# Optimization experiments

Measured on AMD Instinct MI355X. Metric: run time of the kernel, lower is better.

## Reference

```python
import jax, jax.numpy as jnp
import numpy as np

EPS = 1e-12  # torch F.normalize default eps
DN = ('NCHW', 'OIHW', 'NCHW')

def _conv(x, w, groups=1):
    return jax.lax.conv_general_dilated(x, w, window_strides=(1, 1), padding='SAME',
                                        feature_group_count=groups, dimension_numbers=DN)

def setup_inputs() -> dict:
    key = jax.random.key(0)
    k1, k2, k3, k4 = jax.random.split(key, 4)
    b, c, h, w = 4, 64, 64, 64
    x = jax.random.normal(k1, (b, c, h, w), dtype=jnp.float32)
    w_qkv = jax.random.normal(k2, (3 * c, c, 1, 1), dtype=jnp.float32) * (1.0 / np.sqrt(c))
    w_dw = jax.random.normal(k3, (3 * c, 1, 3, 3), dtype=jnp.float32) * (1.0 / 3.0)
    w_proj = jax.random.normal(k4, (c, c, 3, 3), dtype=jnp.float32) * (1.0 / np.sqrt(9 * c))
    return {"x": x, "w_qkv": w_qkv, "w_dw": w_dw, "w_proj": w_proj}

def _l2norm(t):
    # torch F.normalize(dim=-1): t / max(||t||_2, eps)
    n = jnp.sqrt(jnp.sum(t * t, axis=-1, keepdims=True))
    return t / jnp.maximum(n, EPS)

def reference(x, w_qkv, w_dw, w_proj):
    b, c, h, w = x.shape
    qkv = _conv(_conv(x, w_qkv), w_dw, groups=3 * c)  # (b, 3c, h, w)
    q, k, v = jnp.split(qkv, 3, axis=1)
    hw = h * w
    q = _l2norm(q.reshape(b, c, hw))  # normalize each channel's spatial vector
    k = _l2norm(k.reshape(b, c, hw))
    v = v.reshape(b, c, hw)
    attn = jnp.einsum('bcn,bcm->bnm', q, k)        # (b, hw, hw) cosine scores
    attn = jax.nn.softmax(attn, axis=-1)
    out = jnp.einsum('bcm,bmn->bcn', v, attn)       # v @ attn
    out = out.reshape(b, c, h, w)
    return _conv(out, w_proj)
```

## Files before the change

kernel.cpp:

```cpp
#include <hip/hip_runtime.h>
#include <hip/hip_bf16.h>

typedef __attribute__((ext_vector_type(8))) short bf16x8;
typedef __attribute__((ext_vector_type(4))) float f32x4;
typedef __attribute__((ext_vector_type(8))) unsigned short ushort8;

#define HW 4096
#define NC 64
#define PROWS 4356

static __device__ __forceinline__ unsigned short f2bf(float f) {
    unsigned int u = __float_as_uint(f);
    unsigned int r = (u + 0x7FFFu + ((u >> 16) & 1u)) >> 16;
    return (unsigned short)r;
}

__global__ __launch_bounds__(256) void k_conv1x1(const float* __restrict__ x,
                                                 const float* __restrict__ wqkv,
                                                 float* __restrict__ out) {
    __shared__ float wl[512];
    int nb = blockIdx.x, ocg = blockIdx.y, b = blockIdx.z;
    int t = threadIdx.x;
    for (int i = t; i < 512; i += 256) wl[i] = wqkv[ocg * 512 + i];
    __syncthreads();
    int n = nb * 256 + t;
    const float* xb = x + (size_t)b * NC * HW + n;
    float acc[8] = {0.f,0.f,0.f,0.f,0.f,0.f,0.f,0.f};
    for (int ic = 0; ic < 64; ic++) {
        float xv = xb[(size_t)ic * HW];
        #pragma unroll
        for (int o = 0; o < 8; o++) acc[o] += wl[o * 64 + ic] * xv;
    }
    float* ob = out + (size_t)b * 192 * HW + (size_t)(ocg * 8) * HW + n;
    #pragma unroll
    for (int o = 0; o < 8; o++) ob[(size_t)o * HW] = acc[o];
}

__global__ __launch_bounds__(256) void k_dwconv(const float* __restrict__ in,
                                                const float* __restrict__ wdw,
                                                float* __restrict__ out) {
    int yg = blockIdx.x, ch = blockIdx.y, b = blockIdx.z;
    int t = threadIdx.x;
    int y = yg * 4 + (t >> 6), xx = t & 63;
    const float* ib = in + ((size_t)b * 192 + ch) * HW;
    const float* wp = wdw + ch * 9;
    float s = 0.f;
    #pragma unroll
    for (int dy = 0; dy < 3; dy++) {
        int yy = y + dy - 1;
        if (yy < 0 || yy > 63) continue;
        const float* r = ib + yy * 64;
        float v0 = (xx > 0) ? r[xx - 1] : 0.f;
        float v1 = r[xx];
        float v2 = (xx < 63) ? r[xx + 1] : 0.f;
        const float* wr = wp + dy * 3;
        s += wr[0] * v0 + wr[1] * v1 + wr[2] * v2;
    }
    out[((size_t)b * 192 + ch) * HW + y * 64 + xx] = s;
}

__global__ __launch_bounds__(256) void k_norms(const float* __restrict__ qkv,
                                               float* __restrict__ invn) {
    int ch = blockIdx.x, b = blockIdx.y;
    const float* p = qkv + ((size_t)b * 192 + ch) * HW;
    float s = 0.f;
    for (int i = threadIdx.x; i < HW; i += 256) { float v = p[i]; s += v * v; }
    #pragma unroll
    for (int m = 1; m < 64; m <<= 1) s += __shfl_xor(s, m);
    __shared__ float red[4];
    if ((threadIdx.x & 63) == 0) red[threadIdx.x >> 6] = s;
    __syncthreads();
    if (threadIdx.x == 0) {
        float tot = red[0] + red[1] + red[2] + red[3];
        float nrm = sqrtf(tot);
        invn[b * 128 + ch] = 1.f / fmaxf(nrm, 1e-12f);
    }
}

__global__ __launch_bounds__(256) void k_pack(const float* __restrict__ qkv,
                                              const float* __restrict__ invn,
                                              unsigned short* __restrict__ qT,
                                              unsigned short* __restrict__ kT,
                                              unsigned short* __restrict__ vn) {
    int nb = blockIdx.x, sel = blockIdx.y, b = blockIdx.z;
    int n = nb * 256 + threadIdx.x;
    if (sel == 2) {
        const float* src = qkv + ((size_t)b * 192 + 128) * HW + n;
        unsigned short* dst = vn + (size_t)b * NC * HW + n;
        for (int c = 0; c < 64; c++) dst[(size_t)c * HW] = f2bf(src[(size_t)c * HW]);
    } else {
        const float* src = qkv + ((size_t)b * 192 + sel * 64) * HW + n;
        const float* iv = invn + b * 128 + sel * 64;
        unsigned short* dst = (sel == 0 ? qT : kT) + ((size_t)b * HW + n) * NC;
        for (int c0 = 0; c0 < 64; c0 += 8) {
            ushort8 pk;
            #pragma unroll
            for (int j = 0; j < 8; j++)
                pk[j] = f2bf(src[(size_t)(c0 + j) * HW] * iv[c0 + j]);
            *reinterpret_cast<ushort8*>(dst + c0) = pk;
        }
    }
}

__global__ __launch_bounds__(256) void k_rowsum(const unsigned short* __restrict__ qT,
                                                const unsigned short* __restrict__ kT,
                                                float* __restrict__ part) {
    __shared__ __align__(16) unsigned short klds[2][64 * 72];
    int mblk = blockIdx.x, ns = blockIdx.y, b = blockIdx.z;
    int t = threadIdx.x;
    int w = t >> 6, lane = t & 63, g = lane >> 4, r15 = lane & 15;
    const unsigned short* qb = qT + (size_t)b * HW * NC;
    const unsigned short* kb = kT + (size_t)b * HW * NC;
    int m0 = mblk * 128 + w * 16;
    const unsigned short* qp0 = qb + (size_t)(m0 + r15) * NC + g * 8;
    const unsigned short* qp1 = qb + (size_t)(m0 + 64 + r15) * NC + g * 8;
    bf16x8 a0 = *reinterpret_cast<const bf16x8*>(qp0);
    bf16x8 a1 = *reinterpret_cast<const bf16x8*>(qp0 + 32);
    bf16x8 a2 = *reinterpret_cast<const bf16x8*>(qp1);
    bf16x8 a3 = *reinterpret_cast<const bf16x8*>(qp1 + 32);
    float sa[4] = {0.f, 0.f, 0.f, 0.f};
    float sb[4] = {0.f, 0.f, 0.f, 0.f};
    int nbase = ns * 512;
    int n_loc = t >> 2, seg = t & 3;
    {
        const unsigned short* sp = kb + (size_t)(nbase + n_loc) * NC + seg * 16;
        *reinterpret_cast<ushort8*>(&klds[0][n_loc * 72 + seg * 16]) = *reinterpret_cast<const ushort8*>(sp);
        *reinterpret_cast<ushort8*>(&klds[0][n_loc * 72 + seg * 16 + 8]) = *reinterpret_cast<const ushort8*>(sp + 8);
    }
    __syncthreads();
    int cur = 0;
    for (int it = 0; it < 8; it++) {
        ushort8 r0, r1;
        bool hasnext = it < 7;
        if (hasnext) {
            const unsigned short* sp = kb + (size_t)(nbase + (it + 1) * 64 + n_loc) * NC + seg * 16;
            r0 = *reinterpret_cast<const ushort8*>(sp);
            r1 = *reinterpret_cast<const ushort8*>(sp + 8);
        }
        #pragma unroll
        for (int tt = 0; tt < 4; tt++) {
            const unsigned short* kp = &klds[cur][(tt * 16 + r15) * 72 + g * 8];
            bf16x8 b0 = *reinterpret_cast<const bf16x8*>(kp);
            bf16x8 b1 = *reinterpret_cast<const bf16x8*>(kp + 32);
            f32x4 d0 = {0.f, 0.f, 0.f, 0.f};
            f32x4 d1 = {0.f, 0.f, 0.f, 0.f};
            d0 = __builtin_amdgcn_mfma_f32_16x16x32_bf16(a0, b0, d0, 0, 0, 0);
            d1 = __builtin_amdgcn_mfma_f32_16x16x32_bf16(a2, b0, d1, 0, 0, 0);
            d0 = __builtin_amdgcn_mfma_f32_16x16x32_bf16(a1, b1, d0, 0, 0, 0);
            d1 = __builtin_amdgcn_mfma_f32_16x16x32_bf16(a3, b1, d1, 0, 0, 0);
            #pragma unroll
            for (int r = 0; r < 4; r++) { sa[r] += __expf(d0[r]); sb[r] += __expf(d1[r]); }
        }
        if (hasnext) {
            *reinterpret_cast<ushort8*>(&klds[cur ^ 1][n_loc * 72 + seg * 16]) = r0;
            *reinterpret_cast<ushort8*>(&klds[cur ^ 1][n_loc * 72 + seg * 16 + 8]) = r1;
            cur ^= 1;
        }
        __syncthreads();
    }
    #pragma unroll
    for (int off = 1; off < 16; off <<= 1) {
        #pragma unroll
        for (int r = 0; r < 4; r++) {
            sa[r] += __shfl_xor(sa[r], off);
            sb[r] += __shfl_xor(sb[r], off);
        }
    }
    if (r15 == 0) {
        size_t base = ((size_t)ns * 4 + b) * HW;
        f32x4 va = {sa[0], sa[1], sa[2], sa[3]};
        f32x4 vb = {sb[0], sb[1], sb[2], sb[3]};
        *reinterpret_cast<f32x4*>(&part[base + m0 + g * 4]) = va;
        *reinterpret_cast<f32x4*>(&part[base + m0 + 64 + g * 4]) = vb;
    }
}

__global__ __launch_bounds__(256) void k_recip(const float* __restrict__ part,
                                               float* __restrict__ inv) {
    int i = blockIdx.x * 256 + threadIdx.x;
    float s = 0.f;
    #pragma unroll
    for (int ns = 0; ns < 8; ns++) s += part[i + ns * 4 * HW];
    inv[i] = 1.f / s;
}

__global__ __launch_bounds__(256) void k_attn_pv(const unsigned short* __restrict__ qT,
                                                 const unsigned short* __restrict__ kT,
                                                 const unsigned short* __restrict__ vn,
                                                 const float* __restrict__ rowinv,
                                                 float* __restrict__ out4) {
    __shared__ __align__(16) unsigned short klds[64 * 72];
    __shared__ __align__(16) unsigned short plds[2][64 * 72];
    int nblk = blockIdx.x, quarter = blockIdx.y, b = blockIdx.z;
    int t = threadIdx.x;
    int w = t >> 6, lane = t & 63, g = lane >> 4, r15 = lane & 15;
    int n0 = nblk * 64;
    const unsigned short* qb = qT + (size_t)b * HW * NC;
    const unsigned short* kb = kT + (size_t)b * HW * NC;
    const unsigned short* vb = vn + (size_t)b * NC * HW;
    {
        int n_loc = t >> 2, seg = t & 3;
        const unsigned short* sp = kb + (size_t)(n0 + n_loc) * NC + seg * 16;
        *reinterpret_cast<ushort8*>(&klds[n_loc * 72 + seg * 16]) = *reinterpret_cast<const ushort8*>(sp);
        *reinterpret_cast<ushort8*>(&klds[n_loc * 72 + seg * 16 + 8]) = *reinterpret_cast<const ushort8*>(sp + 8);
    }
    __syncthreads();
    f32x4 acc[4] = {{0.f,0.f,0.f,0.f},{0.f,0.f,0.f,0.f},{0.f,0.f,0.f,0.f},{0.f,0.f,0.f,0.f}};
    int mstart = quarter * 1024;
    int mrow = w * 16 + r15;
    {
        const unsigned short* qp = qb + (size_t)(mstart + mrow) * NC + g * 8;
    }
    const unsigned short* qp = qb + (size_t)(mstart + mrow) * NC + g * 8;
    bf16x8 a0 = *reinterpret_cast<const bf16x8*>(qp);
    bf16x8 a1 = *reinterpret_cast<const bf16x8*>(qp + 32);
    float pinv[4];
    #pragma unroll
    for (int r = 0; r < 4; r++)
        pinv[r] = rowinv[(size_t)b * HW + mstart + w * 16 + g * 4 + r];
    int cur = 0;
    for (int mb = mstart; mb < mstart + 1024; mb += 64) {
        const unsigned short* vp = vb + (size_t)mrow * HW + mb + g * 8;
        bf16x8 av0 = *reinterpret_cast<const bf16x8*>(vp);
        bf16x8 av1 = *reinterpret_cast<const bf16x8*>(vp + 32);
        #pragma unroll
        for (int tt = 0; tt < 4; tt++) {
            const unsigned short* kp = &klds[(tt * 16 + r15) * 72 + g * 8];
            bf16x8 b0 = *reinterpret_cast<const bf16x8*>(kp);
            bf16x8 b1 = *reinterpret_cast<const bf16x8*>(kp + 32);
            f32x4 d = {0.f, 0.f, 0.f, 0.f};
            d = __builtin_amdgcn_mfma_f32_16x16x32_bf16(a0, b0, d, 0, 0, 0);
            d = __builtin_amdgcn_mfma_f32_16x16x32_bf16(a1, b1, d, 0, 0, 0);
            unsigned int lo = (unsigned int)f2bf(__expf(d[0]) * pinv[0])
                            | ((unsigned int)f2bf(__expf(d[1]) * pinv[1]) << 16);
            unsigned int hi = (unsigned int)f2bf(__expf(d[2]) * pinv[2])
                            | ((unsigned int)f2bf(__expf(d[3]) * pinv[3]) << 16);
            uint2 pk; pk.x = lo; pk.y = hi;
            *reinterpret_cast<uint2*>(&plds[cur][(tt * 16 + r15) * 72 + w * 16 + g * 4]) = pk;
        }
        bf16x8 a0n = a0, a1n = a1;
        float pinvn[4] = {pinv[0], pinv[1], pinv[2], pinv[3]};
        bool hasnext = (mb + 64) < (mstart + 1024);
        if (hasnext) {
            const unsigned short* qn = qb + (size_t)(mb + 64 + mrow) * NC + g * 8;
            a0n = *reinterpret_cast<const bf16x8*>(qn);
            a1n = *reinterpret_cast<const bf16x8*>(qn + 32);
            #pragma unroll
            for (int r = 0; r < 4; r++)
                pinvn[r] = rowinv[(size_t)b * HW + mb + 64 + w * 16 + g * 4 + r];
        }
        __syncthreads();
        #pragma unroll
        for (int ks = 0; ks < 2; ks++) {
            bf16x8 av = ks ? av1 : av0;
            #pragma unroll
            for (int tt = 0; tt < 4; tt++) {
                bf16x8 bp = *reinterpret_cast<const bf16x8*>(&plds[cur][(tt * 16 + r15) * 72 + ks * 32 + g * 8]);
                acc[tt] = __builtin_amdgcn_mfma_f32_16x16x32_bf16(av, bp, acc[tt], 0, 0, 0);
            }
        }
        a0 = a0n; a1 = a1n;
        #pragma unroll
        for (int r = 0; r < 4; r++) pinv[r] = pinvn[r];
        cur ^= 1;
    }
    float* ob = out4 + ((size_t)quarter * 4 + b) * NC * HW;
    #pragma unroll
    for (int tt = 0; tt < 4; tt++) {
        #pragma unroll
        for (int r = 0; r < 4; r++)
            ob[(size_t)(w * 16 + g * 4 + r) * HW + n0 + tt * 16 + r15] = acc[tt][r];
    }
}

__global__ __launch_bounds__(256) void k_zero(float4* __restrict__ p, int n4) {
    int i = blockIdx.x * 256 + threadIdx.x;
    if (i < n4) p[i] = make_float4(0.f, 0.f, 0.f, 0.f);
}

__global__ __launch_bounds__(256) void k_wconv(const float* __restrict__ wp,
                                               unsigned short* __restrict__ wbf) {
    int idx = blockIdx.x * 256 + threadIdx.x;
    int tap = idx >> 12;
    int rem = idx & 4095;
    int oc = rem >> 6, ic = rem & 63;
    wbf[idx] = f2bf(wp[(oc * 64 + ic) * 9 + tap]);
}

__global__ __launch_bounds__(256) void k_addpack(const float* __restrict__ out4,
                                                 unsigned short* __restrict__ inP) {
    int yb = blockIdx.x, b = blockIdx.y;
    int t = threadIdx.x;
    int x = t & 63, c0 = (t >> 6) * 16;
    int n = yb * 64 + x;
    const float* p0 = out4 + ((size_t)0 * 4 + b) * NC * HW + n;
    const float* p1 = out4 + ((size_t)1 * 4 + b) * NC * HW + n;
    const float* p2 = out4 + ((size_t)2 * 4 + b) * NC * HW + n;
    const float* p3 = out4 + ((size_t)3 * 4 + b) * NC * HW + n;
    unsigned short* dst = inP + ((size_t)b * PROWS + (size_t)(yb + 1) * 66 + 1 + x) * 64 + c0;
    ushort8 v0, v1;
    #pragma unroll
    for (int i = 0; i < 8; i++) {
        size_t o = (size_t)(c0 + i) * HW;
        v0[i] = f2bf(p0[o] + p1[o] + p2[o] + p3[o]);
    }
    #pragma unroll
    for (int i = 0; i < 8; i++) {
        size_t o = (size_t)(c0 + 8 + i) * HW;
        v1[i] = f2bf(p0[o] + p1[o] + p2[o] + p3[o]);
    }
    *reinterpret_cast<ushort8*>(dst) = v0;
    *reinterpret_cast<ushort8*>(dst + 8) = v1;
}

__global__ __launch_bounds__(256) void k_proj_mfma(const unsigned short* __restrict__ inP,
                                                   const unsigned short* __restrict__ wbf,
                                                   float* __restrict__ out) {
    int nb = blockIdx.x, b = blockIdx.y;
    int t = threadIdx.x;
    int w = t >> 6, lane = t & 63, g = lane >> 4, r15 = lane & 15;
    int y = nb >> 1;
    int x0 = (nb & 1) * 32 + (w & 1) * 16;
    int oc0 = (w >> 1) * 32;
    const unsigned short* base = inP + (size_t)b * PROWS * 64;
    f32x4 acc[2] = {{0.f,0.f,0.f,0.f},{0.f,0.f,0.f,0.f}};
    #pragma unroll
    for (int tap = 0; tap < 9; tap++) {
        int dy = tap / 3, dx = tap % 3;
        int p = (y + dy) * 66 + x0 + dx + r15;
        const unsigned short* bp = base + (size_t)p * 64 + g * 8;
        bf16x8 b0 = *reinterpret_cast<const bf16x8*>(bp);
        bf16x8 b1 = *reinterpret_cast<const bf16x8*>(bp + 32);
        #pragma unroll
        for (int tt = 0; tt < 2; tt++) {
            const unsigned short* ap = wbf + tap * 4096 + (size_t)(oc0 + tt * 16 + r15) * 64 + g * 8;
            bf16x8 a0 = *reinterpret_cast<const bf16x8*>(ap);
            bf16x8 a1 = *reinterpret_cast<const bf16x8*>(ap + 32);
            acc[tt] = __builtin_amdgcn_mfma_f32_16x16x32_bf16(a0, b0, acc[tt], 0, 0, 0);
            acc[tt] = __builtin_amdgcn_mfma_f32_16x16x32_bf16(a1, b1, acc[tt], 0, 0, 0);
        }
    }
    int n0 = y * 64 + x0;
    #pragma unroll
    for (int tt = 0; tt < 2; tt++) {
        #pragma unroll
        for (int r = 0; r < 4; r++)
            out[((size_t)b * 64 + oc0 + tt * 16 + g * 4 + r) * HW + n0 + r15] = acc[tt][r];
    }
}

extern "C" void kernel_launch(void* const* d_in, const int* in_sizes, int n_in,
                              void* d_out, int out_size, void* d_ws, size_t ws_size,
                              hipStream_t stream) {
    const float* x    = (const float*)d_in[0];
    const float* wqkv = (const float*)d_in[1];
    const float* wdw  = (const float*)d_in[2];
    const float* wprj = (const float*)d_in[3];
    char* ws = (char*)d_ws;
    float* qkv_raw       = (float*)(ws + 0);
    float* qkv           = (float*)(ws + 12582912);
    unsigned short* qT   = (unsigned short*)(ws + 25165824);
    unsigned short* kT   = (unsigned short*)(ws + 27262976);
    unsigned short* vn   = (unsigned short*)(ws + 29360128);
    float* invn          = (float*)(ws + 31457280);
    float* rowsum_part   = (float*)(ws + 31459328);
    float* rowinv        = (float*)(ws + 31983616);
    unsigned short* wbf  = (unsigned short*)(ws + 32049152);
    unsigned short* inP  = (unsigned short*)(ws + 32122880);
    float* out4          = (float*)(ws + 0);

    int inP4 = (4 * PROWS * 64 * 2) / 16;
    k_zero    <<<dim3((inP4 + 255) / 256), 256, 0, stream>>>((float4*)inP, inP4);
    k_wconv   <<<dim3(144),        256, 0, stream>>>(wprj, wbf);
    k_conv1x1 <<<dim3(16, 24, 4),  256, 0, stream>>>(x, wqkv, qkv_raw);
    k_dwconv  <<<dim3(16, 192, 4), 256, 0, stream>>>(qkv_raw, wdw, qkv);
    k_norms   <<<dim3(128, 4),     256, 0, stream>>>(qkv, invn);
    k_pack    <<<dim3(16, 3, 4),   256, 0, stream>>>(qkv, invn, qT, kT, vn);
    k_rowsum  <<<dim3(32, 8, 4),   256, 0, stream>>>(qT, kT, rowsum_part);
    k_recip   <<<dim3(64),         256, 0, stream>>>(rowsum_part, rowinv);
    k_attn_pv <<<dim3(64, 4, 4),   256, 0, stream>>>(qT, kT, vn, rowinv, out4);
    k_addpack <<<dim3(64, 4),      256, 0, stream>>>(out4, inP);
    k_proj_mfma<<<dim3(128, 4),    256, 0, stream>>>(inP, wbf, (float*)d_out);
}
```

Before: 124.0 us.

## Fuse attention-PV with output packing and switch LDS to XOR swizzle

Replaces the four-way m-split attention kernel plus the separate add-and-pack kernel with one kernel. Each block covers 32 output columns over the full m range and writes bf16 straight into the padded projection input, which removes the fp32 partial-output buffer and its reduction pass. LDS tiles in the rowsum and attention kernels move from padded rows to an XOR-swizzled layout, and bf16 packing uses the v_cvt_pk_bf16_f32 instruction. The grid shrinks to 512 blocks of longer serial loops, which may lower occupancy and latency hiding.

```diff
diff --git a/kernel.cpp b/kernel.cpp
--- a/kernel.cpp
+++ b/kernel.cpp
@@ -105,7 +105,7 @@
 __global__ __launch_bounds__(256) void k_rowsum(const unsigned short* __restrict__ qT,
                                                 const unsigned short* __restrict__ kT,
                                                 float* __restrict__ part) {
-    __shared__ __align__(16) unsigned short klds[2][64 * 72];
+    __shared__ __align__(16) unsigned short klds[2][64 * 64];
     int mblk = blockIdx.x, ns = blockIdx.y, b = blockIdx.z;
     int t = threadIdx.x;
     int w = t >> 6, lane = t & 63, g = lane >> 4, r15 = lane & 15;
@@ -121,27 +121,30 @@
     float sa[4] = {0.f, 0.f, 0.f, 0.f};
     float sb[4] = {0.f, 0.f, 0.f, 0.f};
     int nbase = ns * 512;
-    int n_loc = t >> 2, seg = t & 3;
+    int nl = t >> 2, seg = t & 3;
+    int hs = nl & 7;
+    int c0s = (2 * seg) ^ hs, c1s = (2 * seg + 1) ^ hs;
     {
-        const unsigned short* sp = kb + (size_t)(nbase + n_loc) * NC + seg * 16;
-        *reinterpret_cast<ushort8*>(&klds[0][n_loc * 72 + seg * 16]) = *reinterpret_cast<const ushort8*>(sp);
-        *reinterpret_cast<ushort8*>(&klds[0][n_loc * 72 + seg * 16 + 8]) = *reinterpret_cast<const ushort8*>(sp + 8);
+        const unsigned short* sp = kb + (size_t)(nbase + nl) * NC + seg * 16;
+        *reinterpret_cast<ushort8*>(&klds[0][nl * 64 + c0s * 8]) = *reinterpret_cast<const ushort8*>(sp);
+        *reinterpret_cast<ushort8*>(&klds[0][nl * 64 + c1s * 8]) = *reinterpret_cast<const ushort8*>(sp + 8);
     }
     __syncthreads();
     int cur = 0;
+    int hr = r15 & 7;
     for (int it = 0; it < 8; it++) {
         ushort8 r0, r1;
         bool hasnext = it < 7;
         if (hasnext) {
-            const unsigned short* sp = kb + (size_t)(nbase + (it + 1) * 64 + n_loc) * NC + seg * 16;
+            const unsigned short* sp = kb + (size_t)(nbase + (it + 1) * 64 + nl) * NC + seg * 16;
             r0 = *reinterpret_cast<const ushort8*>(sp);
             r1 = *reinterpret_cast<const ushort8*>(sp + 8);
         }
         #pragma unroll
         for (int tt = 0; tt < 4; tt++) {
-            const unsigned short* kp = &klds[cur][(tt * 16 + r15) * 72 + g * 8];
-            bf16x8 b0 = *reinterpret_cast<const bf16x8*>(kp);
-            bf16x8 b1 = *reinterpret_cast<const bf16x8*>(kp + 32);
+            int row = tt * 16 + r15;
+            bf16x8 b0 = *reinterpret_cast<const bf16x8*>(&klds[cur][row * 64 + ((g    ) ^ hr) * 8]);
+            bf16x8 b1 = *reinterpret_cast<const bf16x8*>(&klds[cur][row * 64 + ((g + 4) ^ hr) * 8]);
             f32x4 d0 = {0.f, 0.f, 0.f, 0.f};
             f32x4 d1 = {0.f, 0.f, 0.f, 0.f};
             d0 = __builtin_amdgcn_mfma_f32_16x16x32_bf16(a0, b0, d0, 0, 0, 0);
@@ -152,8 +155,8 @@
             for (int r = 0; r < 4; r++) { sa[r] += __expf(d0[r]); sb[r] += __expf(d1[r]); }
         }
         if (hasnext) {
-            *reinterpret_cast<ushort8*>(&klds[cur ^ 1][n_loc * 72 + seg * 16]) = r0;
-            *reinterpret_cast<ushort8*>(&klds[cur ^ 1][n_loc * 72 + seg * 16 + 8]) = r1;
+            *reinterpret_cast<ushort8*>(&klds[cur ^ 1][nl * 64 + c0s * 8]) = r0;
+            *reinterpret_cast<ushort8*>(&klds[cur ^ 1][nl * 64 + c1s * 8]) = r1;
             cur ^= 1;
         }
         __syncthreads();
@@ -184,92 +187,97 @@
     inv[i] = 1.f / s;
 }
 
-__global__ __launch_bounds__(256) void k_attn_pv(const unsigned short* __restrict__ qT,
-                                                 const unsigned short* __restrict__ kT,
-                                                 const unsigned short* __restrict__ vn,
-                                                 const float* __restrict__ rowinv,
-                                                 float* __restrict__ out4) {
-    __shared__ __align__(16) unsigned short klds[64 * 72];
-    __shared__ __align__(16) unsigned short plds[2][64 * 72];
-    int nblk = blockIdx.x, quarter = blockIdx.y, b = blockIdx.z;
+__global__ __launch_bounds__(256) void k_attn_fused(const unsigned short* __restrict__ qT,
+                                                    const unsigned short* __restrict__ kT,
+                                                    const unsigned short* __restrict__ vn,
+                                                    const float* __restrict__ rowinv,
+                                                    unsigned short* __restrict__ inP) {
+    __shared__ __align__(16) unsigned short klds[32 * 64];
+    __shared__ __align__(16) unsigned short plds[2][32 * 64];
+    int nb = blockIdx.x, b = blockIdx.y;
     int t = threadIdx.x;
     int w = t >> 6, lane = t & 63, g = lane >> 4, r15 = lane & 15;
-    int n0 = nblk * 64;
+    int n0 = nb * 32;
     const unsigned short* qb = qT + (size_t)b * HW * NC;
     const unsigned short* kb = kT + (size_t)b * HW * NC;
     const unsigned short* vb = vn + (size_t)b * NC * HW;
+    const float* rib = rowinv + (size_t)b * HW;
     {
-        int n_loc = t >> 2, seg = t & 3;
-        const unsigned short* sp = kb + (size_t)(n0 + n_loc) * NC + seg * 16;
-        *reinterpret_cast<ushort8*>(&klds[n_loc * 72 + seg * 16]) = *reinterpret_cast<const ushort8*>(sp);
-        *reinterpret_cast<ushort8*>(&klds[n_loc * 72 + seg * 16 + 8]) = *reinterpret_cast<const ushort8*>(sp + 8);
+        int nl = t >> 3, ck = t & 7;
+        ushort8 v = *reinterpret_cast<const ushort8*>(kb + (size_t)(n0 + nl) * NC + ck * 8);
+        *reinterpret_cast<ushort8*>(&klds[nl * 64 + (ck ^ (nl & 7)) * 8]) = v;
     }
     __syncthreads();
-    f32x4 acc[4] = {{0.f,0.f,0.f,0.f},{0.f,0.f,0.f,0.f},{0.f,0.f,0.f,0.f},{0.f,0.f,0.f,0.f}};
-    int mstart = quarter * 1024;
+    f32x4 acc[2] = {{0.f,0.f,0.f,0.f},{0.f,0.f,0.f,0.f}};
     int mrow = w * 16 + r15;
-    {
-        const unsigned short* qp = qb + (size_t)(mstart + mrow) * NC + g * 8;
-    }
-    const unsigned short* qp = qb + (size_t)(mstart + mrow) * NC + g * 8;
-    bf16x8 a0 = *reinterpret_cast<const bf16x8*>(qp);
-    bf16x8 a1 = *reinterpret_cast<const bf16x8*>(qp + 32);
+    int hr = r15 & 7;
+    const unsigned short* qp = qb + (size_t)mrow * NC + g * 8;
+    bf16x8 qa0 = *reinterpret_cast<const bf16x8*>(qp);
+    bf16x8 qa1 = *reinterpret_cast<const bf16x8*>(qp + 32);
+    const unsigned short* vrow = vb + (size_t)mrow * HW;
+    bf16x8 va0 = *reinterpret_cast<const bf16x8*>(vrow + g * 8);
+    bf16x8 va1 = *reinterpret_cast<const bf16x8*>(vrow + 32 + g * 8);
     float pinv[4];
     #pragma unroll
-    for (int r = 0; r < 4; r++)
-        pinv[r] = rowinv[(size_t)b * HW + mstart + w * 16 + g * 4 + r];
+    for (int r = 0; r < 4; r++) pinv[r] = rib[w * 16 + g * 4 + r];
     int cur = 0;
-    for (int mb = mstart; mb < mstart + 1024; mb += 64) {
-        const unsigned short* vp = vb + (size_t)mrow * HW + mb + g * 8;
-        bf16x8 av0 = *reinterpret_cast<const bf16x8*>(vp);
-        bf16x8 av1 = *reinterpret_cast<const bf16x8*>(vp + 32);
-        #pragma unroll
-        for (int tt = 0; tt < 4; tt++) {
-            const unsigned short* kp = &klds[(tt * 16 + r15) * 72 + g * 8];
-            bf16x8 b0 = *reinterpret_cast<const bf16x8*>(kp);
-            bf16x8 b1 = *reinterpret_cast<const bf16x8*>(kp + 32);
+    for (int it = 0; it < 64; it++) {
+        int mb = it * 64;
+        #pragma unroll
+        for (int tt = 0; tt < 2; tt++) {
+            int row = tt * 16 + r15;
+            bf16x8 b0 = *reinterpret_cast<const bf16x8*>(&klds[row * 64 + ((g    ) ^ hr) * 8]);
+            bf16x8 b1 = *reinterpret_cast<const bf16x8*>(&klds[row * 64 + ((g + 4) ^ hr) * 8]);
             f32x4 d = {0.f, 0.f, 0.f, 0.f};
-            d = __builtin_amdgcn_mfma_f32_16x16x32_bf16(a0, b0, d, 0, 0, 0);
-            d = __builtin_amdgcn_mfma_f32_16x16x32_bf16(a1, b1, d, 0, 0, 0);
-            unsigned int lo = (unsigned int)f2bf(__expf(d[0]) * pinv[0])
-                            | ((unsigned int)f2bf(__expf(d[1]) * pinv[1]) << 16);
-            unsigned int hi = (unsigned int)f2bf(__expf(d[2]) * pinv[2])
-                            | ((unsigned int)f2bf(__expf(d[3]) * pinv[3]) << 16);
+            d = __builtin_amdgcn_mfma_f32_16x16x32_bf16(qa0, b0, d, 0, 0, 0);
+            d = __builtin_amdgcn_mfma_f32_16x16x32_bf16(qa1, b1, d, 0, 0, 0);
+            float p0 = __expf(d[0]) * pinv[0];
+            float p1 = __expf(d[1]) * pinv[1];
+            float p2 = __expf(d[2]) * pinv[2];
+            float p3 = __expf(d[3]) * pinv[3];
+            unsigned int lo, hi;
+            asm("v_cvt_pk_bf16_f32 %0, %1, %2" : "=v"(lo) : "v"(p0), "v"(p1));
+            asm("v_cvt_pk_bf16_f32 %0, %1, %2" : "=v"(hi) : "v"(p2), "v"(p3));
+            int ck = (2 * w + (g >> 1)) ^ hr;
             uint2 pk; pk.x = lo; pk.y = hi;
-            *reinterpret_cast<uint2*>(&plds[cur][(tt * 16 + r15) * 72 + w * 16 + g * 4]) = pk;
-        }
-        bf16x8 a0n = a0, a1n = a1;
+            *reinterpret_cast<uint2*>(
+                reinterpret_cast<char*>(&plds[cur][row * 64]) + ck * 16 + (g & 1) * 8) = pk;
+        }
+        bf16x8 qn0 = qa0, qn1 = qa1, vn0 = va0, vn1 = va1;
         float pinvn[4] = {pinv[0], pinv[1], pinv[2], pinv[3]};
-        bool hasnext = (mb + 64) < (mstart + 1024);
-        if (hasnext) {
+        if (it < 63) {
             const unsigned short* qn = qb + (size_t)(mb + 64 + mrow) * NC + g * 8;
-            a0n = *reinterpret_cast<const bf16x8*>(qn);
-            a1n = *reinterpret_cast<const bf16x8*>(qn + 32);
+            qn0 = *reinterpret_cast<const bf16x8*>(qn);
+            qn1 = *reinterpret_cast<const bf16x8*>(qn + 32);
+            vn0 = *reinterpret_cast<const bf16x8*>(vrow + mb + 64 + g * 8);
+            vn1 = *reinterpret_cast<const bf16x8*>(vrow + mb + 96 + g * 8);
             #pragma unroll
-            for (int r = 0; r < 4; r++)
-                pinvn[r] = rowinv[(size_t)b * HW + mb + 64 + w * 16 + g * 4 + r];
+            for (int r = 0; r < 4; r++) pinvn[r] = rib[mb + 64 + w * 16 + g * 4 + r];
         }
         __syncthreads();
         #pragma unroll
-        for (int ks = 0; ks < 2; ks++) {
-            bf16x8 av = ks ? av1 : av0;
-            #pragma unroll
-            for (int tt = 0; tt < 4; tt++) {
-                bf16x8 bp = *reinterpret_cast<const bf16x8*>(&plds[cur][(tt * 16 + r15) * 72 + ks * 32 + g * 8]);
-                acc[tt] = __builtin_amdgcn_mfma_f32_16x16x32_bf16(av, bp, acc[tt], 0, 0, 0);
-            }
-        }
-        a0 = a0n; a1 = a1n;
+        for (int tt = 0; tt < 2; tt++) {
+            int row = tt * 16 + r15;
+            bf16x8 p0 = *reinterpret_cast<const bf16x8*>(&plds[cur][row * 64 + ((g    ) ^ hr) * 8]);
+            bf16x8 p1 = *reinterpret_cast<const bf16x8*>(&plds[cur][row * 64 + ((g + 4) ^ hr) * 8]);
+            acc[tt] = __builtin_amdgcn_mfma_f32_16x16x32_bf16(va0, p0, acc[tt], 0, 0, 0);
+            acc[tt] = __builtin_amdgcn_mfma_f32_16x16x32_bf16(va1, p1, acc[tt], 0, 0, 0);
+        }
+        qa0 = qn0; qa1 = qn1; va0 = vn0; va1 = vn1;
         #pragma unroll
         for (int r = 0; r < 4; r++) pinv[r] = pinvn[r];
         cur ^= 1;
     }
-    float* ob = out4 + ((size_t)quarter * 4 + b) * NC * HW;
-    #pragma unroll
-    for (int tt = 0; tt < 4; tt++) {
-        #pragma unroll
-        for (int r = 0; r < 4; r++)
-            ob[(size_t)(w * 16 + g * 4 + r) * HW + n0 + tt * 16 + r15] = acc[tt][r];
+    int y = nb >> 1;
+    #pragma unroll
+    for (int tt = 0; tt < 2; tt++) {
+        int x = (nb & 1) * 32 + tt * 16 + r15;
+        unsigned short* dst = inP + ((size_t)b * PROWS + (size_t)(y + 1) * 66 + 1 + x) * 64 + w * 16 + g * 4;
+        unsigned int lo, hi;
+        asm("v_cvt_pk_bf16_f32 %0, %1, %2" : "=v"(lo) : "v"(acc[tt][0]), "v"(acc[tt][1]));
+        asm("v_cvt_pk_bf16_f32 %0, %1, %2" : "=v"(hi) : "v"(acc[tt][2]), "v"(acc[tt][3]));
+        uint2 pk; pk.x = lo; pk.y = hi;
+        *reinterpret_cast<uint2*>(dst) = pk;
     }
 }
 
@@ -285,32 +293,6 @@
     int rem = idx & 4095;
     int oc = rem >> 6, ic = rem & 63;
     wbf[idx] = f2bf(wp[(oc * 64 + ic) * 9 + tap]);
-}
-
-__global__ __launch_bounds__(256) void k_addpack(const float* __restrict__ out4,
-                                                 unsigned short* __restrict__ inP) {
-    int yb = blockIdx.x, b = blockIdx.y;
-    int t = threadIdx.x;
-    int x = t & 63, c0 = (t >> 6) * 16;
-    int n = yb * 64 + x;
-    const float* p0 = out4 + ((size_t)0 * 4 + b) * NC * HW + n;
-    const float* p1 = out4 + ((size_t)1 * 4 + b) * NC * HW + n;
-    const float* p2 = out4 + ((size_t)2 * 4 + b) * NC * HW + n;
-    const float* p3 = out4 + ((size_t)3 * 4 + b) * NC * HW + n;
-    unsigned short* dst = inP + ((size_t)b * PROWS + (size_t)(yb + 1) * 66 + 1 + x) * 64 + c0;
-    ushort8 v0, v1;
-    #pragma unroll
-    for (int i = 0; i < 8; i++) {
-        size_t o = (size_t)(c0 + i) * HW;
-        v0[i] = f2bf(p0[o] + p1[o] + p2[o] + p3[o]);
-    }
-    #pragma unroll
-    for (int i = 0; i < 8; i++) {
-        size_t o = (size_t)(c0 + 8 + i) * HW;
-        v1[i] = f2bf(p0[o] + p1[o] + p2[o] + p3[o]);
-    }
-    *reinterpret_cast<ushort8*>(dst) = v0;
-    *reinterpret_cast<ushort8*>(dst + 8) = v1;
 }
 
 __global__ __launch_bounds__(256) void k_proj_mfma(const unsigned short* __restrict__ inP,
@@ -367,18 +349,16 @@
     float* rowinv        = (float*)(ws + 31983616);
     unsigned short* wbf  = (unsigned short*)(ws + 32049152);
     unsigned short* inP  = (unsigned short*)(ws + 32122880);
-    float* out4          = (float*)(ws + 0);
 
     int inP4 = (4 * PROWS * 64 * 2) / 16;
-    k_zero    <<<dim3((inP4 + 255) / 256), 256, 0, stream>>>((float4*)inP, inP4);
-    k_wconv   <<<dim3(144),        256, 0, stream>>>(wprj, wbf);
-    k_conv1x1 <<<dim3(16, 24, 4),  256, 0, stream>>>(x, wqkv, qkv_raw);
-    k_dwconv  <<<dim3(16, 192, 4), 256, 0, stream>>>(qkv_raw, wdw, qkv);
-    k_norms   <<<dim3(128, 4),     256, 0, stream>>>(qkv, invn);
-    k_pack    <<<dim3(16, 3, 4),   256, 0, stream>>>(qkv, invn, qT, kT, vn);
-    k_rowsum  <<<dim3(32, 8, 4),   256, 0, stream>>>(qT, kT, rowsum_part);
-    k_recip   <<<dim3(64),         256, 0, stream>>>(rowsum_part, rowinv);
-    k_attn_pv <<<dim3(64, 4, 4),   256, 0, stream>>>(qT, kT, vn, rowinv, out4);
-    k_addpack <<<dim3(64, 4),      256, 0, stream>>>(out4, inP);
-    k_proj_mfma<<<dim3(128, 4),    256, 0, stream>>>(inP, wbf, (float*)d_out);
-}
+    k_zero       <<<dim3((inP4 + 255) / 256), 256, 0, stream>>>((float4*)inP, inP4);
+    k_wconv      <<<dim3(144),        256, 0, stream>>>(wprj, wbf);
+    k_conv1x1    <<<dim3(16, 24, 4),  256, 0, stream>>>(x, wqkv, qkv_raw);
+    k_dwconv     <<<dim3(16, 192, 4), 256, 0, stream>>>(qkv_raw, wdw, qkv);
+    k_norms      <<<dim3(128, 4),     256, 0, stream>>>(qkv, invn);
+    k_pack       <<<dim3(16, 3, 4),   256, 0, stream>>>(qkv, invn, qT, kT, vn);
+    k_rowsum     <<<dim3(32, 8, 4),   256, 0, stream>>>(qT, kT, rowsum_part);
+    k_recip      <<<dim3(64),         256, 0, stream>>>(rowsum_part, rowinv);
+    k_attn_fused <<<dim3(128, 4),     256, 0, stream>>>(qT, kT, vn, rowinv, inP);
+    k_proj_mfma  <<<dim3(128, 4),     256, 0, stream>>>(inP, wbf, (float*)d_out);
+}
```

Result: slower. 143.6 us (+15.8%).
